# Kernel optimization log

Hardware: AMD Instinct MI355X
Metric: run time of the kernel (lower is better)

## Reference

```python
import jax, jax.numpy as jnp
import numpy as np

B, S, D = 4, 2048, 1024


def setup_inputs() -> dict:
    key = jax.random.key(0)
    kx, kq, kk, kv, km = jax.random.split(key, 5)
    x = jax.random.normal(kx, (B, S, D), dtype=jnp.float32)
    # bias-free Linear weights, torch convention W: (out, in), y = x @ W.T
    Wq = jax.random.normal(kq, (D, D), dtype=jnp.float32) * 0.02
    Wk = jax.random.normal(kk, (D, D), dtype=jnp.float32) * 0.02
    Wv = jax.random.normal(kv, (D, D), dtype=jnp.float32) * 0.02
    # quantum mask: probability vector per batch over seq positions
    q_mask = jax.nn.softmax(jax.random.normal(km, (B, S), dtype=jnp.float32), axis=-1)
    return {"x": x, "Wq": Wq, "Wk": Wk, "Wv": Wv, "q_mask": q_mask}


def reference(x, Wq, Wk, Wv, q_mask):
    # projections (torch Linear: x @ W.T)
    q = jnp.einsum("bsd,ed->bse", x, Wq)
    k = jnp.einsum("bsd,ed->bse", x, Wk)
    v = jnp.einsum("bsd,ed->bse", x, Wv)
    scale = 1.0 / jnp.sqrt(jnp.asarray(D, dtype=x.dtype))
    scores = jnp.einsum("bqe,bke->bqk", q, k) * scale  # (B, S, S)
    # per-row multiplicative quantum mask (mask broadcast over key dim)
    scores = scores * q_mask[:, :, None]
    attn = jax.nn.softmax(scores, axis=-1)
    out = jnp.einsum("bqk,bkd->bqd", attn, v)
    return out
```

## Files before the change

### kernel.cpp

```cpp
#include <hip/hip_runtime.h>
#include <hip/hip_bf16.h>

#define BB 4
#define SS 2048
#define DD 1024

using f32x4  = __attribute__((ext_vector_type(4))) float;
using f32x16 = __attribute__((ext_vector_type(16))) float;
using i32x4  = __attribute__((ext_vector_type(4))) int;
using i32x8  = __attribute__((ext_vector_type(8))) int;

struct f8_t { unsigned char b; };

__device__ __forceinline__ void gld16(const void* g, void* l) {
    __builtin_amdgcn_global_load_lds(
        (const __attribute__((address_space(1))) void*)(g),
        (__attribute__((address_space(3))) void*)(l),
        16, 0, 0);
}

__device__ __forceinline__ void store1(float* p, float v) { *p = v; }
__device__ __forceinline__ void store1(f8_t* p, float v)  {
    p->b = (unsigned char)(__builtin_amdgcn_cvt_pk_fp8_f32(v, v, 0, false) & 0xff);
}

__global__ void cvt_x_xsum_kernel(const float* __restrict__ x,
                                  unsigned char* __restrict__ x8,
                                  float* __restrict__ xsum) {
    int b  = blockIdx.x >> 6;
    int s0 = (blockIdx.x & 63) * 32;
    int t  = threadIdx.x;
    int g  = t >> 7;
    int dt = t & 127;
    int d8 = dt * 8;
    const float* xb = x + ((size_t)b * SS + s0 + g * 16) * DD + d8;
    unsigned char* x8b = x8 + ((size_t)b * SS + s0 + g * 16) * DD + d8;

    float a0=0,a1=0,a2=0,a3=0,a4=0,a5=0,a6=0,a7=0;
#pragma unroll 4
    for (int i = 0; i < 16; ++i) {
        float4 u = *(const float4*)(xb + (size_t)i * DD);
        float4 v = *(const float4*)(xb + (size_t)i * DD + 4);
        int lo = __builtin_amdgcn_cvt_pk_fp8_f32(u.x, u.y, 0, false);
        lo     = __builtin_amdgcn_cvt_pk_fp8_f32(u.z, u.w, lo, true);
        int hi = __builtin_amdgcn_cvt_pk_fp8_f32(v.x, v.y, 0, false);
        hi     = __builtin_amdgcn_cvt_pk_fp8_f32(v.z, v.w, hi, true);
        *(int2*)(x8b + (size_t)i * DD) = make_int2(lo, hi);
        a0 += u.x; a1 += u.y; a2 += u.z; a3 += u.w;
        a4 += v.x; a5 += v.y; a6 += v.z; a7 += v.w;
    }
    __shared__ float red[2][128][8];
    float* r = red[g][dt];
    r[0]=a0; r[1]=a1; r[2]=a2; r[3]=a3; r[4]=a4; r[5]=a5; r[6]=a6; r[7]=a7;
    __syncthreads();
    if (t < 128) {
        float* p0 = red[0][t];
        float* p1 = red[1][t];
#pragma unroll
        for (int j = 0; j < 8; ++j)
            atomicAdd(&xsum[b * DD + t * 8 + j], p0[j] + p1[j]);
    }
}

__global__ void cvt_w_kernel(const float* __restrict__ Wq, const float* __restrict__ Wk,
                             const float* __restrict__ Wv, unsigned char* __restrict__ w8, int n8) {
    int i = blockIdx.x * blockDim.x + threadIdx.x;
    int seg = i / n8;
    int j = i - seg * n8;
    const float* src = (seg == 0) ? Wq : (seg == 1) ? Wk : Wv;
    float4 a = ((const float4*)src)[2 * j];
    float4 b = ((const float4*)src)[2 * j + 1];
    int lo = __builtin_amdgcn_cvt_pk_fp8_f32(a.x, a.y, 0, false);
    lo     = __builtin_amdgcn_cvt_pk_fp8_f32(a.z, a.w, lo, true);
    int hi = __builtin_amdgcn_cvt_pk_fp8_f32(b.x, b.y, 0, false);
    hi     = __builtin_amdgcn_cvt_pk_fp8_f32(b.z, b.w, hi, true);
    ((int2*)(w8 + (size_t)seg * n8 * 8))[j] = make_int2(lo, hi);
}

__global__ void colsumv_kernel(const float* __restrict__ Wv, const float* __restrict__ xsum,
                               float* __restrict__ colsum) {
    int idx  = blockIdx.x * 4 + (threadIdx.x >> 6);
    int b    = idx >> 10, c = idx & 1023;
    int lane = threadIdx.x & 63;
    const float* wr = Wv + (size_t)c * DD;
    const float* xs = xsum + b * DD;
    float acc = 0.f;
#pragma unroll 4
    for (int d = lane; d < DD; d += 64) acc += wr[d] * xs[d];
#pragma unroll
    for (int off = 32; off; off >>= 1) acc += __shfl_xor(acc, off);
    if (lane == 0) colsum[idx] = acc;
}

template <int MODE, typename CT>
__global__ __launch_bounds__(256, 2) void gemm_f8(
    const unsigned char* __restrict__ A, const unsigned char* __restrict__ B,
    CT* __restrict__ C, int M, int N, int K,
    long batchA, long batchB, long batchC,
    int ldc, int col_shift, long cstride,
    const float* __restrict__ qmask, float* __restrict__ rsum,
    const float* __restrict__ colsum) {
    constexpr int BM = 128, BN = 128, BK = 256;
    constexpr int SCALE_A = (MODE == 3) ? 118 : 127;
    __shared__ __attribute__((aligned(16))) unsigned char As[BM * BK];
    __shared__ __attribute__((aligned(16))) unsigned char Bs[BN * BK];

    const int tid  = threadIdx.x;
    const int lane = tid & 63;
    const int wv   = tid >> 6;
    const int l31  = lane & 31;
    const int half = lane >> 5;
    const int hb   = half * 2;
    const int wm   = wv >> 1;
    const int wn   = wv & 1;

    const int m0 = blockIdx.y * BM;
    const int n0 = blockIdx.x * BN;
    const long z = blockIdx.z;
    const unsigned char* Ab = A + z * batchA;
    const unsigned char* Bb = B + z * batchB;

    f32x16 acc[2][2] = {};

#define STAGE(dst, src, kt, j) do {                                           \
        int slot_ = (j) * 256 + tid;                                          \
        int r_ = slot_ >> 4;                                                  \
        int c_ = (slot_ & 15) ^ (r_ & 7);                                     \
        gld16((src) + (size_t)r_ * K + ((kt) + c_ * 16),                      \
              (dst) + (size_t)((j) * 256 + wv * 64) * 16);                    \
    } while (0)
#define RDFRAG(f, base, rr, s) do {                                           \
        int r_ = (rr);                                                        \
        int c0_ = (s) * 4 + hb;                                               \
        const unsigned char* rp_ = (base) + r_ * 256;                         \
        i32x4 q0_ = *(const i32x4*)(rp_ + ((c0_ ^ (r_ & 7)) * 16));           \
        i32x4 q1_ = *(const i32x4*)(rp_ + (((c0_ + 1) ^ (r_ & 7)) * 16));     \
        f[0]=q0_[0]; f[1]=q0_[1]; f[2]=q0_[2]; f[3]=q0_[3];                   \
        f[4]=q1_[0]; f[5]=q1_[1]; f[6]=q1_[2]; f[7]=q1_[3];                   \
    } while (0)
#define MFMA(d, a, b) \
        d = __builtin_amdgcn_mfma_scale_f32_32x32x64_f8f6f4(a, b, d, 0, 0, 0, SCALE_A, 0, 127)

    for (int kt = 0; kt < K; kt += BK) {
        const unsigned char* Asrc = Ab + (size_t)m0 * K;
        const unsigned char* Bsrc = Bb + (size_t)n0 * K;
        STAGE(As, Asrc, kt, 0); STAGE(As, Asrc, kt, 1);
        STAGE(As, Asrc, kt, 2); STAGE(As, Asrc, kt, 3);
        STAGE(As, Asrc, kt, 4); STAGE(As, Asrc, kt, 5);
        STAGE(As, Asrc, kt, 6); STAGE(As, Asrc, kt, 7);
        STAGE(Bs, Bsrc, kt, 0); STAGE(Bs, Bsrc, kt, 1);
        STAGE(Bs, Bsrc, kt, 2); STAGE(Bs, Bsrc, kt, 3);
        STAGE(Bs, Bsrc, kt, 4); STAGE(Bs, Bsrc, kt, 5);
        STAGE(Bs, Bsrc, kt, 6); STAGE(Bs, Bsrc, kt, 7);
        asm volatile("s_waitcnt vmcnt(0)" ::: "memory");
        __syncthreads();

#pragma unroll
        for (int s = 0; s < 4; ++s) {
            i32x8 a0, a1, b0, b1;
            RDFRAG(a0, As, wm * 64 +  0 + l31, s);
            RDFRAG(a1, As, wm * 64 + 32 + l31, s);
            RDFRAG(b0, Bs, wn * 64 +  0 + l31, s);
            RDFRAG(b1, Bs, wn * 64 + 32 + l31, s);
            MFMA(acc[0][0], a0, b0); MFMA(acc[0][1], a0, b1);
            MFMA(acc[1][0], a1, b0); MFMA(acc[1][1], a1, b1);
        }
        __syncthreads();
    }
#undef STAGE
#undef RDFRAG
#undef MFMA

    CT* Cb = C + z * batchC;

    if constexpr (MODE == 0) {
#pragma unroll
        for (int mi = 0; mi < 2; ++mi)
#pragma unroll
            for (int ni = 0; ni < 2; ++ni) {
                int colg = n0 + wn * 64 + ni * 32 + l31;
#pragma unroll
                for (int reg = 0; reg < 16; ++reg) {
                    int rowg = m0 + wm * 64 + mi * 32 + (reg & 3) + 8 * (reg >> 2) + 4 * half;
                    store1(Cb + (size_t)rowg * ldc + colg, acc[mi][ni][reg]);
                }
            }
    } else if constexpr (MODE == 1) {
#pragma unroll
        for (int mi = 0; mi < 2; ++mi)
#pragma unroll
            for (int ni = 0; ni < 2; ++ni) {
                int colg = n0 + wn * 64 + ni * 32 + l31;
                int cb   = colg >> col_shift;
                int ccol = colg - (cb << col_shift);
#pragma unroll
                for (int reg = 0; reg < 16; ++reg) {
                    int rowg = m0 + wm * 64 + mi * 32 + (reg & 3) + 8 * (reg >> 2) + 4 * half;
                    store1(Cb + (long)cb * cstride + (size_t)rowg * ldc + ccol, acc[mi][ni][reg]);
                }
            }
    } else if constexpr (MODE == 2) {
        const float* qm = qmask + (z << 11);
        float* rs = rsum + (z << 11);
#pragma unroll
        for (int mi = 0; mi < 2; ++mi) {
#pragma unroll
            for (int reg = 0; reg < 16; ++reg) {
                int rowg = m0 + wm * 64 + mi * 32 + (reg & 3) + 8 * (reg >> 2) + 4 * half;
                float fac = qm[rowg] * 0.03125f;
                float part = 0.f;
#pragma unroll
                for (int ni = 0; ni < 2; ++ni) {
                    int colg = n0 + wn * 64 + ni * 32 + l31;
                    float t = __expf(acc[mi][ni][reg] * fac) - 1.0f;
                    part += t;
                    store1(Cb + (size_t)rowg * ldc + colg, t * 512.0f);
                }
                part += __shfl_xor(part, 1);
                part += __shfl_xor(part, 2);
                part += __shfl_xor(part, 4);
                part += __shfl_xor(part, 8);
                part += __shfl_xor(part, 16);
                if (l31 == 0) atomicAdd(&rs[rowg], part);
            }
        }
    } else {
        const float* rs = rsum + (z << 11);
        const float* cs = colsum + (z << 10);
#pragma unroll
        for (int mi = 0; mi < 2; ++mi) {
#pragma unroll
            for (int reg = 0; reg < 16; ++reg) {
                int rowg = m0 + wm * 64 + mi * 32 + (reg & 3) + 8 * (reg >> 2) + 4 * half;
                float inv = 1.0f / (2048.0f + rs[rowg]);
#pragma unroll
                for (int ni = 0; ni < 2; ++ni) {
                    int colg = n0 + wn * 64 + ni * 32 + l31;
                    store1(Cb + (size_t)rowg * ldc + colg, (acc[mi][ni][reg] + cs[colg]) * inv);
                }
            }
        }
    }
}

extern "C" void kernel_launch(void* const* d_in, const int* in_sizes, int n_in,
                              void* d_out, int out_size, void* d_ws, size_t ws_size,
                              hipStream_t stream) {
    const float* x     = (const float*)d_in[0];
    const float* Wq    = (const float*)d_in[1];
    const float* Wk    = (const float*)d_in[2];
    const float* Wv    = (const float*)d_in[3];
    const float* qmask = (const float*)d_in[4];
    float* out = (float*)d_out;

    const long nx = (long)BB * SS * DD;
    const long nw = (long)DD * DD;

    unsigned char* ws  = (unsigned char*)d_ws;
    unsigned char* x8  = ws;
    unsigned char* w8  = x8 + nx;
    unsigned char* qk8 = w8 + 3 * nw;
    unsigned char* vt8 = qk8 + 2 * nx;
    unsigned char* t8  = vt8 + nx;
    float* xsum   = (float*)(t8 + (long)BB * SS * SS);
    float* rs     = xsum + BB * DD;
    float* colsum = rs + BB * SS;

    hipMemsetAsync(xsum, 0, (size_t)(BB * DD + BB * SS) * sizeof(float), stream);

    cvt_x_xsum_kernel<<<dim3(256), dim3(256), 0, stream>>>(x, x8, xsum);
    cvt_w_kernel<<<dim3((int)(3 * nw / 8 / 256)), dim3(256), 0, stream>>>(Wq, Wk, Wv, w8, (int)(nw / 8));
    colsumv_kernel<<<dim3(1024), dim3(256), 0, stream>>>(Wv, xsum, colsum);

    gemm_f8<0, f8_t><<<dim3(DD / 128, (BB * SS) / 128, 2), 256, 0, stream>>>(
        x8, w8, (f8_t*)qk8, BB * SS, DD, DD, 0, nw, nx, DD, 31, 0, nullptr, nullptr, nullptr);

    gemm_f8<1, f8_t><<<dim3((BB * SS) / 128, DD / 128, 1), 256, 0, stream>>>(
        w8 + 2 * nw, x8, (f8_t*)vt8, DD, BB * SS, DD, 0, 0, 0, SS, 11, (long)DD * SS,
        nullptr, nullptr, nullptr);

    gemm_f8<2, f8_t><<<dim3(SS / 128, SS / 128, BB), 256, 0, stream>>>(
        qk8, qk8 + nx, (f8_t*)t8, SS, SS, DD, (long)SS * DD, (long)SS * DD, (long)SS * SS,
        SS, 31, 0, qmask, rs, nullptr);

    gemm_f8<3, float><<<dim3(DD / 128, SS / 128, BB), 256, 0, stream>>>(
        t8, vt8, out, SS, DD, SS, (long)SS * SS, (long)DD * SS, (long)SS * DD,
        DD, 31, 0, nullptr, rs, colsum);
}
```

Measured before the change: 233.1 us.

## Fuse QKV projections and colsum into one launch, halve GEMM K-tile

Merges the memset into the weight-convert kernel and folds the Q/K projection, V-transpose projection, and V column-sum kernels into a single launch that dispatches on a linear block index. The GEMM K-tile drops from 256 to 128, which cuts LDS per block to 32KB so launch bounds can allow 4 blocks per CU instead of 2. The aim is fewer launches and higher occupancy for latency hiding. The cost is twice as many K iterations, each with its own barriers and unoverlapped loads.

```diff
diff --git a/kernel.cpp b/kernel.cpp
--- a/kernel.cpp
+++ b/kernel.cpp
@@ -22,6 +22,26 @@
 __device__ __forceinline__ void store1(float* p, float v) { *p = v; }
 __device__ __forceinline__ void store1(f8_t* p, float v)  {
     p->b = (unsigned char)(__builtin_amdgcn_cvt_pk_fp8_f32(v, v, 0, false) & 0xff);
+}
+
+__global__ void cvt_w_zero(const float* __restrict__ Wq, const float* __restrict__ Wk,
+                           const float* __restrict__ Wv, unsigned char* __restrict__ w8,
+                           int n8, float* __restrict__ zbuf) {
+    if (blockIdx.x == 1536) {
+        for (int i = threadIdx.x; i < 12288; i += 256) zbuf[i] = 0.f;
+        return;
+    }
+    int i = blockIdx.x * blockDim.x + threadIdx.x;
+    int seg = i / n8;
+    int j = i - seg * n8;
+    const float* src = (seg == 0) ? Wq : (seg == 1) ? Wk : Wv;
+    float4 a = ((const float4*)src)[2 * j];
+    float4 b = ((const float4*)src)[2 * j + 1];
+    int lo = __builtin_amdgcn_cvt_pk_fp8_f32(a.x, a.y, 0, false);
+    lo     = __builtin_amdgcn_cvt_pk_fp8_f32(a.z, a.w, lo, true);
+    int hi = __builtin_amdgcn_cvt_pk_fp8_f32(b.x, b.y, 0, false);
+    hi     = __builtin_amdgcn_cvt_pk_fp8_f32(b.z, b.w, hi, true);
+    ((int2*)(w8 + (size_t)seg * n8 * 8))[j] = make_int2(lo, hi);
 }
 
 __global__ void cvt_x_xsum_kernel(const float* __restrict__ x,
@@ -62,26 +82,13 @@
     }
 }
 
-__global__ void cvt_w_kernel(const float* __restrict__ Wq, const float* __restrict__ Wk,
-                             const float* __restrict__ Wv, unsigned char* __restrict__ w8, int n8) {
-    int i = blockIdx.x * blockDim.x + threadIdx.x;
-    int seg = i / n8;
-    int j = i - seg * n8;
-    const float* src = (seg == 0) ? Wq : (seg == 1) ? Wk : Wv;
-    float4 a = ((const float4*)src)[2 * j];
-    float4 b = ((const float4*)src)[2 * j + 1];
-    int lo = __builtin_amdgcn_cvt_pk_fp8_f32(a.x, a.y, 0, false);
-    lo     = __builtin_amdgcn_cvt_pk_fp8_f32(a.z, a.w, lo, true);
-    int hi = __builtin_amdgcn_cvt_pk_fp8_f32(b.x, b.y, 0, false);
-    hi     = __builtin_amdgcn_cvt_pk_fp8_f32(b.z, b.w, hi, true);
-    ((int2*)(w8 + (size_t)seg * n8 * 8))[j] = make_int2(lo, hi);
-}
-
-__global__ void colsumv_kernel(const float* __restrict__ Wv, const float* __restrict__ xsum,
-                               float* __restrict__ colsum) {
-    int idx  = blockIdx.x * 4 + (threadIdx.x >> 6);
+__device__ __forceinline__ void colsumv_body(const float* __restrict__ Wv,
+                                             const float* __restrict__ xsum,
+                                             float* __restrict__ colsum,
+                                             int vb, int tid) {
+    int idx  = vb * 4 + (tid >> 6);
     int b    = idx >> 10, c = idx & 1023;
-    int lane = threadIdx.x & 63;
+    int lane = tid & 63;
     const float* wr = Wv + (size_t)c * DD;
     const float* xs = xsum + b * DD;
     float acc = 0.f;
@@ -93,17 +100,18 @@
 }
 
 template <int MODE, typename CT>
-__global__ __launch_bounds__(256, 2) void gemm_f8(
+__device__ __forceinline__ void gemm_body(
     const unsigned char* __restrict__ A, const unsigned char* __restrict__ B,
-    CT* __restrict__ C, int M, int N, int K,
+    CT* __restrict__ C, int K,
     long batchA, long batchB, long batchC,
     int ldc, int col_shift, long cstride,
     const float* __restrict__ qmask, float* __restrict__ rsum,
-    const float* __restrict__ colsum) {
-    constexpr int BM = 128, BN = 128, BK = 256;
+    const float* __restrict__ colsum,
+    int bx, int by, long z, unsigned char* smem) {
+    constexpr int BM = 128, BN = 128, BK = 128;
     constexpr int SCALE_A = (MODE == 3) ? 118 : 127;
-    __shared__ __attribute__((aligned(16))) unsigned char As[BM * BK];
-    __shared__ __attribute__((aligned(16))) unsigned char Bs[BN * BK];
+    unsigned char* As = smem;
+    unsigned char* Bs = smem + 16384;
 
     const int tid  = threadIdx.x;
     const int lane = tid & 63;
@@ -114,9 +122,8 @@
     const int wm   = wv >> 1;
     const int wn   = wv & 1;
 
-    const int m0 = blockIdx.y * BM;
-    const int n0 = blockIdx.x * BN;
-    const long z = blockIdx.z;
+    const int m0 = by * BM;
+    const int n0 = bx * BN;
     const unsigned char* Ab = A + z * batchA;
     const unsigned char* Bb = B + z * batchB;
 
@@ -124,15 +131,15 @@
 
 #define STAGE(dst, src, kt, j) do {                                           \
         int slot_ = (j) * 256 + tid;                                          \
-        int r_ = slot_ >> 4;                                                  \
-        int c_ = (slot_ & 15) ^ (r_ & 7);                                     \
+        int r_ = slot_ >> 3;                                                  \
+        int c_ = (slot_ & 7) ^ (r_ & 7);                                      \
         gld16((src) + (size_t)r_ * K + ((kt) + c_ * 16),                      \
               (dst) + (size_t)((j) * 256 + wv * 64) * 16);                    \
     } while (0)
 #define RDFRAG(f, base, rr, s) do {                                           \
         int r_ = (rr);                                                        \
         int c0_ = (s) * 4 + hb;                                               \
-        const unsigned char* rp_ = (base) + r_ * 256;                         \
+        const unsigned char* rp_ = (base) + r_ * 128;                         \
         i32x4 q0_ = *(const i32x4*)(rp_ + ((c0_ ^ (r_ & 7)) * 16));           \
         i32x4 q1_ = *(const i32x4*)(rp_ + (((c0_ + 1) ^ (r_ & 7)) * 16));     \
         f[0]=q0_[0]; f[1]=q0_[1]; f[2]=q0_[2]; f[3]=q0_[3];                   \
@@ -146,17 +153,13 @@
         const unsigned char* Bsrc = Bb + (size_t)n0 * K;
         STAGE(As, Asrc, kt, 0); STAGE(As, Asrc, kt, 1);
         STAGE(As, Asrc, kt, 2); STAGE(As, Asrc, kt, 3);
-        STAGE(As, Asrc, kt, 4); STAGE(As, Asrc, kt, 5);
-        STAGE(As, Asrc, kt, 6); STAGE(As, Asrc, kt, 7);
         STAGE(Bs, Bsrc, kt, 0); STAGE(Bs, Bsrc, kt, 1);
         STAGE(Bs, Bsrc, kt, 2); STAGE(Bs, Bsrc, kt, 3);
-        STAGE(Bs, Bsrc, kt, 4); STAGE(Bs, Bsrc, kt, 5);
-        STAGE(Bs, Bsrc, kt, 6); STAGE(Bs, Bsrc, kt, 7);
         asm volatile("s_waitcnt vmcnt(0)" ::: "memory");
         __syncthreads();
 
 #pragma unroll
-        for (int s = 0; s < 4; ++s) {
+        for (int s = 0; s < 2; ++s) {
             i32x8 a0, a1, b0, b1;
             RDFRAG(a0, As, wm * 64 +  0 + l31, s);
             RDFRAG(a1, As, wm * 64 + 32 + l31, s);
@@ -243,6 +246,44 @@
     }
 }
 
+__global__ __launch_bounds__(256, 4) void fused_qkvc(
+    const unsigned char* __restrict__ x8, const unsigned char* __restrict__ w8,
+    unsigned char* __restrict__ qk8, unsigned char* __restrict__ vt8,
+    const float* __restrict__ Wv, const float* __restrict__ xsum,
+    float* __restrict__ colsum) {
+    extern __shared__ unsigned char smem[];
+    const long nx = (long)BB * SS * DD;
+    const long nw = (long)DD * DD;
+    int lin = blockIdx.x;
+    if (lin < 2048) {
+        long z = lin >> 10;
+        int r  = lin & 1023;
+        gemm_body<0, f8_t>(x8, w8, (f8_t*)qk8, DD, 0, nw, nx, DD, 31, 0,
+                           nullptr, nullptr, nullptr, r & 7, r >> 3, z, smem);
+    } else if (lin < 2560) {
+        int r = lin - 2048;
+        gemm_body<1, f8_t>(w8 + 2 * nw, x8, (f8_t*)vt8, DD, 0, 0, 0, SS, 11,
+                           (long)DD * SS, nullptr, nullptr, nullptr,
+                           r & 63, r >> 6, 0, smem);
+    } else {
+        colsumv_body(Wv, xsum, colsum, lin - 2560, threadIdx.x);
+    }
+}
+
+template <int MODE, typename CT>
+__global__ __launch_bounds__(256, 4) void gemm_k(
+    const unsigned char* __restrict__ A, const unsigned char* __restrict__ B,
+    CT* __restrict__ C, int K,
+    long batchA, long batchB, long batchC,
+    int ldc, int col_shift, long cstride,
+    const float* __restrict__ qmask, float* __restrict__ rsum,
+    const float* __restrict__ colsum) {
+    extern __shared__ unsigned char smem[];
+    gemm_body<MODE, CT>(A, B, C, K, batchA, batchB, batchC, ldc, col_shift,
+                        cstride, qmask, rsum, colsum,
+                        blockIdx.x, blockIdx.y, blockIdx.z, smem);
+}
+
 extern "C" void kernel_launch(void* const* d_in, const int* in_sizes, int n_in,
                               void* d_out, int out_size, void* d_ws, size_t ws_size,
                               hipStream_t stream) {
@@ -266,24 +307,17 @@
     float* rs     = xsum + BB * DD;
     float* colsum = rs + BB * SS;
 
-    hipMemsetAsync(xsum, 0, (size_t)(BB * DD + BB * SS) * sizeof(float), stream);
+    cvt_w_zero<<<dim3(1537), dim3(256), 0, stream>>>(Wq, Wk, Wv, w8, (int)(nw / 8), xsum);
 
     cvt_x_xsum_kernel<<<dim3(256), dim3(256), 0, stream>>>(x, x8, xsum);
-    cvt_w_kernel<<<dim3((int)(3 * nw / 8 / 256)), dim3(256), 0, stream>>>(Wq, Wk, Wv, w8, (int)(nw / 8));
-    colsumv_kernel<<<dim3(1024), dim3(256), 0, stream>>>(Wv, xsum, colsum);
-
-    gemm_f8<0, f8_t><<<dim3(DD / 128, (BB * SS) / 128, 2), 256, 0, stream>>>(
-        x8, w8, (f8_t*)qk8, BB * SS, DD, DD, 0, nw, nx, DD, 31, 0, nullptr, nullptr, nullptr);
-
-    gemm_f8<1, f8_t><<<dim3((BB * SS) / 128, DD / 128, 1), 256, 0, stream>>>(
-        w8 + 2 * nw, x8, (f8_t*)vt8, DD, BB * SS, DD, 0, 0, 0, SS, 11, (long)DD * SS,
-        nullptr, nullptr, nullptr);
-
-    gemm_f8<2, f8_t><<<dim3(SS / 128, SS / 128, BB), 256, 0, stream>>>(
-        qk8, qk8 + nx, (f8_t*)t8, SS, SS, DD, (long)SS * DD, (long)SS * DD, (long)SS * SS,
+
+    fused_qkvc<<<dim3(3584), dim3(256), 32768, stream>>>(x8, w8, qk8, vt8, Wv, xsum, colsum);
+
+    gemm_k<2, f8_t><<<dim3(SS / 128, SS / 128, BB), dim3(256), 32768, stream>>>(
+        qk8, qk8 + nx, (f8_t*)t8, DD, (long)SS * DD, (long)SS * DD, (long)SS * SS,
         SS, 31, 0, qmask, rs, nullptr);
 
-    gemm_f8<3, float><<<dim3(DD / 128, SS / 128, BB), 256, 0, stream>>>(
-        t8, vt8, out, SS, DD, SS, (long)SS * SS, (long)DD * SS, (long)SS * DD,
+    gemm_k<3, float><<<dim3(DD / 128, SS / 128, BB), dim3(256), 32768, stream>>>(
+        t8, vt8, out, SS, (long)SS * SS, (long)DD * SS, (long)SS * DD,
         DD, 31, 0, nullptr, rs, colsum);
 }
```

Measured after the change: 225.5 us. 1.03x faster.
